# Performance work log

Hardware: AMD Instinct MI355X
Metric: run time of the kernel (lower is better)

## Reference

```python
import jax, jax.numpy as jnp
import numpy as np

B, S, D, H, HD, F = 2, 2048, 2048, 16, 128, 8192
EPS = 1e-6
NEG_INF = -1e10


def rmsnorm(x, scale, eps=EPS):
    # T5 LayerNorm: no centering, mean of squares, learned scale
    x = x.astype(jnp.float32)
    mean2 = jnp.mean(jnp.square(x), axis=-1, keepdims=True)
    return x * jax.lax.rsqrt(mean2 + eps) * scale


def setup_inputs() -> dict:
    key = jax.random.key(0)
    ks = jax.random.split(key, 10)
    sd = 0.02
    return {
        "x": jax.random.normal(ks[0], (B, S, D), jnp.float32),
        "ln1_scale": jnp.ones((D,), jnp.float32),
        "wq": jax.random.normal(ks[1], (D, H, HD), jnp.float32) * sd,
        "wk": jax.random.normal(ks[2], (D, H, HD), jnp.float32) * sd,
        "wv": jax.random.normal(ks[3], (D, H, HD), jnp.float32) * sd,
        "qln_scale": jnp.ones((HD,), jnp.float32),
        "kln_scale": jnp.ones((HD,), jnp.float32),
        "wo": jax.random.normal(ks[4], (H, HD, D), jnp.float32) * sd,
        "ln2_scale": jnp.ones((D,), jnp.float32),
        "wi0": jax.random.normal(ks[5], (D, F), jnp.float32) * sd,
        "wi1": jax.random.normal(ks[6], (D, F), jnp.float32) * sd,
        "wout": jax.random.normal(ks[7], (F, D), jnp.float32) * sd,
    }


def reference(x, ln1_scale, wq, wk, wv, qln_scale, kln_scale, wo, ln2_scale, wi0, wi1, wout):
    # ---- pre-attention RMSNorm ----
    lnx = rmsnorm(x, ln1_scale)                                  # [B,S,D]
    # ---- QKV projections (DenseGeneral D -> (H,HD)) ----
    q = jnp.einsum("bsd,dhk->bshk", lnx, wq)                      # [B,S,H,HD]
    k = jnp.einsum("bsd,dhk->bshk", lnx, wk)
    v = jnp.einsum("bsd,dhk->bshk", lnx, wv)
    # ---- fused per-head QK LayerNorm ----
    q = rmsnorm(q, qln_scale)
    k = rmsnorm(k, kln_scale)
    # ---- attention scores + causal bias + softmax ----
    logits = jnp.einsum("bqhd,bkhd->bhqk", q, k)                  # [B,H,S,S]
    causal = jnp.tril(jnp.ones((S, S), bool))
    bias = jnp.where(causal, 0.0, NEG_INF).astype(logits.dtype)  # [S,S]
    probs = jax.nn.softmax(logits + bias[None, None])             # [B,H,S,S]
    # ---- weighted values + output projection ----
    attn = jnp.einsum("bhqk,bkhd->bqhd", probs, v)                # [B,S,H,HD]
    attn_out = jnp.einsum("bqhd,hdm->bqm", attn, wo)              # [B,S,D]
    inter = x + attn_out
    # ---- pre-MLP RMSNorm + gated MLP (silu * linear) ----
    h = rmsnorm(inter, ln2_scale)
    g = jax.nn.silu(h @ wi0) * (h @ wi1)                          # [B,S,F]
    mlp_out = g @ wout                                            # [B,S,D]
    return inter + mlp_out
```

## Files before the change

kernel.cpp:

```cpp
#include <hip/hip_runtime.h>

typedef unsigned short u16;
typedef unsigned int u32;
typedef __attribute__((ext_vector_type(8))) short bf16x8;
typedef __attribute__((ext_vector_type(2))) float f32x2;
typedef __attribute__((ext_vector_type(4))) float f32x4;
typedef __attribute__((ext_vector_type(4))) u32 u32x4;
typedef __attribute__((ext_vector_type(4))) unsigned short u16x4;

#define DEV __device__ __forceinline__

DEV u16 f2bf(float x) {
    u32 u = __builtin_bit_cast(u32, x);
    u += 0x7fffu + ((u >> 16) & 1u);
    return (u16)(u >> 16);
}
DEV float bf2f(u16 b) {
    u32 u = ((u32)b) << 16;
    return __builtin_bit_cast(float, u);
}

#define MFMA16(a, b, c) __builtin_amdgcn_mfma_f32_16x16x32_bf16((a), (b), (c), 0, 0, 0)

#define GLL16(gp, lp)                                                      \
    __builtin_amdgcn_global_load_lds(                                      \
        (const __attribute__((address_space(1))) u32*)(const void*)(gp),   \
        (__attribute__((address_space(3))) u32*)(void*)(lp), 16, 0, 0)

__global__ void fillsent(float* __restrict__ out, int n, float val)
{
    for (int i = blockIdx.x * blockDim.x + threadIdx.x; i < n; i += gridDim.x * blockDim.x)
        out[i] = val;
}

__global__ void wtrans(const float* __restrict__ in, u16* __restrict__ out, int K, int N)
{
    __shared__ u16 t[64][66];
    const int n0 = blockIdx.x * 64, k0 = blockIdx.y * 64, tid = threadIdx.x;
#pragma unroll
    for (int i = 0; i < 4; ++i) {
        int e = (i * 256 + tid) * 4;
        int r = e >> 6, c = e & 63;
        f32x4 v = *(const f32x4*)&in[(size_t)(k0 + r) * N + n0 + c];
        t[r][c] = f2bf(v[0]); t[r][c + 1] = f2bf(v[1]);
        t[r][c + 2] = f2bf(v[2]); t[r][c + 3] = f2bf(v[3]);
    }
    __syncthreads();
#pragma unroll
    for (int i = 0; i < 4; ++i) {
        int e = (i * 256 + tid) * 4;
        int r = e >> 6, c = e & 63;
        u16x4 wv;
        wv[0] = t[c][r]; wv[1] = t[c + 1][r]; wv[2] = t[c + 2][r]; wv[3] = t[c + 3][r];
        *(u16x4*)&out[(size_t)(n0 + r) * K + k0 + c] = wv;
    }
}

__global__ void wtrans4(const float* __restrict__ s0, const float* __restrict__ s1,
                        const float* __restrict__ s2, const float* __restrict__ s3,
                        u16* __restrict__ d0, u16* __restrict__ d1,
                        u16* __restrict__ d2, u16* __restrict__ d3)
{
    const float* in;
    u16* out;
    switch (blockIdx.z) {
        case 0: in = s0; out = d0; break;
        case 1: in = s1; out = d1; break;
        case 2: in = s2; out = d2; break;
        default: in = s3; out = d3; break;
    }
    __shared__ u16 t[64][66];
    const int n0 = blockIdx.x * 64, k0 = blockIdx.y * 64, tid = threadIdx.x;
#pragma unroll
    for (int i = 0; i < 4; ++i) {
        int e = (i * 256 + tid) * 4;
        int r = e >> 6, c = e & 63;
        f32x4 v = *(const f32x4*)&in[(size_t)(k0 + r) * 2048 + n0 + c];
        t[r][c] = f2bf(v[0]); t[r][c + 1] = f2bf(v[1]);
        t[r][c + 2] = f2bf(v[2]); t[r][c + 3] = f2bf(v[3]);
    }
    __syncthreads();
#pragma unroll
    for (int i = 0; i < 4; ++i) {
        int e = (i * 256 + tid) * 4;
        int r = e >> 6, c = e & 63;
        u16x4 wv;
        wv[0] = t[c][r]; wv[1] = t[c + 1][r]; wv[2] = t[c + 2][r]; wv[3] = t[c + 3][r];
        *(u16x4*)&out[(size_t)(n0 + r) * 2048 + k0 + c] = wv;
    }
}

__global__ void vtrans(const u16* __restrict__ in, u16* __restrict__ out)
{
    __shared__ u16 t[64][65];
    const int d0 = blockIdx.x * 64, s0 = blockIdx.y * 64, bh = blockIdx.z, tid = threadIdx.x;
    const u16* ip = in + (size_t)bh * 2048 * 128;
    u16* op = out + (size_t)bh * 128 * 2048;
    for (int i = tid; i < 4096; i += 256) {
        int r = i >> 6, c = i & 63;
        t[r][c] = ip[(size_t)(s0 + r) * 128 + d0 + c];
    }
    __syncthreads();
    for (int i = tid; i < 4096; i += 256) {
        int r = i >> 6, c = i & 63;
        op[(size_t)(d0 + r) * 2048 + s0 + c] = t[c][r];
    }
}

__global__ __launch_bounds__(256) void rmsnorm_d(const float* __restrict__ in,
                                                 const float* __restrict__ sc,
                                                 u16* __restrict__ out)
{
    __shared__ float red[4];
    const int row = blockIdx.x, tid = threadIdx.x;
    const float* p = in + (size_t)row * 2048 + tid * 8;
    f32x4 a = *(const f32x4*)p;
    f32x4 b = *(const f32x4*)(p + 4);
    float ss = a[0]*a[0] + a[1]*a[1] + a[2]*a[2] + a[3]*a[3]
             + b[0]*b[0] + b[1]*b[1] + b[2]*b[2] + b[3]*b[3];
    for (int d = 1; d < 64; d <<= 1) ss += __shfl_xor(ss, d, 64);
    if ((tid & 63) == 0) red[tid >> 6] = ss;
    __syncthreads();
    float rs = rsqrtf((red[0] + red[1] + red[2] + red[3]) * (1.0f / 2048.0f) + 1e-6f);
    const float* s = sc + tid * 8;
    u32x4 ov;
#pragma unroll
    for (int i = 0; i < 2; ++i) {
        f32x4 v = i ? b : a;
#pragma unroll
        for (int j = 0; j < 2; ++j) {
            float v0 = v[j * 2] * rs * s[i * 4 + j * 2];
            float v1 = v[j * 2 + 1] * rs * s[i * 4 + j * 2 + 1];
            ov[i * 2 + j] = (u32)f2bf(v0) | ((u32)f2bf(v1) << 16);
        }
    }
    *(u32x4*)(out + (size_t)row * 2048 + tid * 8) = ov;
}

__global__ __launch_bounds__(256) void rmsnorm_split(const float* __restrict__ in,
                                                     const float* __restrict__ sc,
                                                     u16* __restrict__ ohi,
                                                     u16* __restrict__ olo)
{
    __shared__ float red[4];
    const int row = blockIdx.x, tid = threadIdx.x;
    const float* p = in + (size_t)row * 2048 + tid * 8;
    f32x4 a = *(const f32x4*)p;
    f32x4 b = *(const f32x4*)(p + 4);
    float ss = a[0]*a[0] + a[1]*a[1] + a[2]*a[2] + a[3]*a[3]
             + b[0]*b[0] + b[1]*b[1] + b[2]*b[2] + b[3]*b[3];
    for (int d = 1; d < 64; d <<= 1) ss += __shfl_xor(ss, d, 64);
    if ((tid & 63) == 0) red[tid >> 6] = ss;
    __syncthreads();
    float rs = rsqrtf((red[0] + red[1] + red[2] + red[3]) * (1.0f / 2048.0f) + 1e-6f);
    const float* s = sc + tid * 8;
    u32x4 oh, ol;
#pragma unroll
    for (int i = 0; i < 2; ++i) {
        f32x4 v = i ? b : a;
#pragma unroll
        for (int j = 0; j < 2; ++j) {
            float v0 = v[j * 2] * rs * s[i * 4 + j * 2];
            float v1 = v[j * 2 + 1] * rs * s[i * 4 + j * 2 + 1];
            u16 h0 = f2bf(v0), h1 = f2bf(v1);
            u16 l0 = f2bf(v0 - bf2f(h0)), l1 = f2bf(v1 - bf2f(h1));
            oh[i * 2 + j] = (u32)h0 | ((u32)h1 << 16);
            ol[i * 2 + j] = (u32)l0 | ((u32)l1 << 16);
        }
    }
    *(u32x4*)(ohi + (size_t)row * 2048 + tid * 8) = oh;
    *(u32x4*)(olo + (size_t)row * 2048 + tid * 8) = ol;
}

template <int EPI>
__global__ __launch_bounds__(512, 2)
void gemm_bt8(const u16* __restrict__ Ap, const u16* __restrict__ Bt,
              float* __restrict__ outf, u16* __restrict__ outb,
              const float* __restrict__ resf, int M, int N, int K)
{
    extern __shared__ char lds[];
    char* AB = lds;
    char* BB = lds + 49152;
    const int tid = threadIdx.x, w = tid >> 6, l = tid & 63;
    const int lr = l & 15, lg = l >> 4;
    const int m0 = blockIdx.y * 128, n0 = blockIdx.x * 256;
    const int wr = (w >> 2) * 64, wc = (w & 3) * 64;
    const size_t ldb = (size_t)K * 2;
    const char* Ag = (const char*)Ap;
    const char* Bg = (const char*)Bt;
    const int ldsw = w * 1024;

    size_t ago[2], bgo[4];
#pragma unroll
    for (int i = 0; i < 2; ++i) {
        int p = (i * 512 + tid) * 16;
        int pr = p >> 7;
        int pc = (p ^ ((pr & 7) << 4)) & 127;
        ago[i] = (size_t)(m0 + pr) * ldb + pc;
    }
#pragma unroll
    for (int i = 0; i < 4; ++i) {
        int p = (i * 512 + tid) * 16;
        int pr = p >> 7;
        int pc = (p ^ ((pr & 7) << 4)) & 127;
        bgo[i] = (size_t)(n0 + pr) * ldb + pc;
    }

    f32x4 acc[4][4] = {};
    const int nkt = K / 64;

    GLL16(Ag + ago[0], AB + ldsw);
    GLL16(Ag + ago[1], AB + 8192 + ldsw);
    GLL16(Bg + bgo[0], BB + ldsw);
    GLL16(Bg + bgo[1], BB + 8192 + ldsw);
    GLL16(Bg + bgo[2], BB + 16384 + ldsw);
    GLL16(Bg + bgo[3], BB + 24576 + ldsw);
    if (nkt > 1) {
        char* Ad = AB + 16384;
        char* Bd = BB + 32768;
        GLL16(Ag + ago[0] + 128, Ad + ldsw);
        GLL16(Ag + ago[1] + 128, Ad + 8192 + ldsw);
        GLL16(Bg + bgo[0] + 128, Bd + ldsw);
        GLL16(Bg + bgo[1] + 128, Bd + 8192 + ldsw);
        GLL16(Bg + bgo[2] + 128, Bd + 16384 + ldsw);
        GLL16(Bg + bgo[3] + 128, Bd + 24576 + ldsw);
        asm volatile("s_waitcnt vmcnt(6)" ::: "memory");
    } else {
        asm volatile("s_waitcnt vmcnt(0)" ::: "memory");
    }
    __builtin_amdgcn_s_barrier();

    int cur = 0, stg = 2;
    for (int kt = 0; kt < nkt; ++kt) {
        char* Ac = AB + cur * 16384;
        char* Bc = BB + cur * 32768;
        char* Asd = AB + stg * 16384;
        char* Bsd = BB + stg * 32768;
        const bool dost = (kt + 2 < nkt);
        const size_t koff = (size_t)(kt + 2) * 128;

        bf16x8 af[4], bfa, bfb;
#pragma unroll
        for (int mf = 0; mf < 4; ++mf) {
            int ra = wr + mf * 16 + lr;
            af[mf] = *(const bf16x8*)(Ac + ((ra * 128 + lg * 16) ^ ((ra & 7) << 4)));
        }
        {
            int rb = wc + lr;
            bfa = *(const bf16x8*)(Bc + ((rb * 128 + lg * 16) ^ ((rb & 7) << 4)));
            rb = wc + 16 + lr;
            bfb = *(const bf16x8*)(Bc + ((rb * 128 + lg * 16) ^ ((rb & 7) << 4)));
        }
        if (dost) {
            GLL16(Ag + ago[0] + koff, Asd + ldsw);
            GLL16(Ag + ago[1] + koff, Asd + 8192 + ldsw);
        }
        __builtin_amdgcn_s_barrier();
        __builtin_amdgcn_s_setprio(1);
#pragma unroll
        for (int mf = 0; mf < 4; ++mf) acc[mf][0] = MFMA16(af[mf], bfa, acc[mf][0]);
#pragma unroll
        for (int mf = 0; mf < 4; ++mf) acc[mf][1] = MFMA16(af[mf], bfb, acc[mf][1]);
        __builtin_amdgcn_s_setprio(0);
        __builtin_amdgcn_s_barrier();
        {
            int rb = wc + 32 + lr;
            bfa = *(const bf16x8*)(Bc + ((rb * 128 + lg * 16) ^ ((rb & 7) << 4)));
            rb = wc + 48 + lr;
            bfb = *(const bf16x8*)(Bc + ((rb * 128 + lg * 16) ^ ((rb & 7) << 4)));
        }
        if (dost) {
            GLL16(Bg + bgo[0] + koff, Bsd + ldsw);
            GLL16(Bg + bgo[1] + koff, Bsd + 8192 + ldsw);
        }
        __builtin_amdgcn_s_barrier();
        __builtin_amdgcn_s_setprio(1);
#pragma unroll
        for (int mf = 0; mf < 4; ++mf) acc[mf][2] = MFMA16(af[mf], bfa, acc[mf][2]);
#pragma unroll
        for (int mf = 0; mf < 4; ++mf) acc[mf][3] = MFMA16(af[mf], bfb, acc[mf][3]);
        __builtin_amdgcn_s_setprio(0);
        __builtin_amdgcn_s_barrier();
#pragma unroll
        for (int mf = 0; mf < 4; ++mf) {
            int ra = wr + mf * 16 + lr;
            af[mf] = *(const bf16x8*)(Ac + ((ra * 128 + 64 + lg * 16) ^ ((ra & 7) << 4)));
        }
        {
            int rb = wc + lr;
            bfa = *(const bf16x8*)(Bc + ((rb * 128 + 64 + lg * 16) ^ ((rb & 7) << 4)));
            rb = wc + 16 + lr;
            bfb = *(const bf16x8*)(Bc + ((rb * 128 + 64 + lg * 16) ^ ((rb & 7) << 4)));
        }
        if (dost) {
            GLL16(Bg + bgo[2] + koff, Bsd + 16384 + ldsw);
        }
        __builtin_amdgcn_s_barrier();
        __builtin_amdgcn_s_setprio(1);
#pragma unroll
        for (int mf = 0; mf < 4; ++mf) acc[mf][0] = MFMA16(af[mf], bfa, acc[mf][0]);
#pragma unroll
        for (int mf = 0; mf < 4; ++mf) acc[mf][1] = MFMA16(af[mf], bfb, acc[mf][1]);
        __builtin_amdgcn_s_setprio(0);
        __builtin_amdgcn_s_barrier();
        {
            int rb = wc + 32 + lr;
            bfa = *(const bf16x8*)(Bc + ((rb * 128 + 64 + lg * 16) ^ ((rb & 7) << 4)));
            rb = wc + 48 + lr;
            bfb = *(const bf16x8*)(Bc + ((rb * 128 + 64 + lg * 16) ^ ((rb & 7) << 4)));
        }
        if (dost) {
            GLL16(Bg + bgo[3] + koff, Bsd + 24576 + ldsw);
        }
        __builtin_amdgcn_s_barrier();
        __builtin_amdgcn_s_setprio(1);
#pragma unroll
        for (int mf = 0; mf < 4; ++mf) acc[mf][2] = MFMA16(af[mf], bfa, acc[mf][2]);
#pragma unroll
        for (int mf = 0; mf < 4; ++mf) acc[mf][3] = MFMA16(af[mf], bfb, acc[mf][3]);
        __builtin_amdgcn_s_setprio(0);
        if (kt < nkt - 2) {
            asm volatile("s_waitcnt vmcnt(6)" ::: "memory");
            __builtin_amdgcn_s_barrier();
        } else if (kt == nkt - 2) {
            asm volatile("s_waitcnt vmcnt(0)" ::: "memory");
            __builtin_amdgcn_s_barrier();
        }
        cur = (cur == 2) ? 0 : cur + 1;
        stg = (stg == 2) ? 0 : stg + 1;
    }

#pragma unroll
    for (int mf = 0; mf < 4; ++mf) {
#pragma unroll
        for (int nf = 0; nf < 4; ++nf) {
#pragma unroll
            for (int r = 0; r < 4; ++r) {
                int m = m0 + wr + mf * 16 + lg * 4 + r;
                int n = n0 + wc + nf * 16 + lr;
                float v = acc[mf][nf][r];
                if constexpr (EPI == 0) {
                    outb[(((m >> 11) * 16 + (n >> 7)) << 18) + ((m & 2047) << 7) + (n & 127)] = f2bf(v);
                } else {
                    size_t idx = (size_t)m * N + n;
                    outf[idx] = v + resf[idx];
                }
            }
        }
    }
}

__global__ __launch_bounds__(256, 2)
void gemm2qk(const u16* __restrict__ Ahi, const u16* __restrict__ Alo,
             const u16* __restrict__ Bq, const u16* __restrict__ Bk,
             const float* __restrict__ qsc, const float* __restrict__ ksc,
             u16* __restrict__ qhi, u16* __restrict__ qlo,
             u16* __restrict__ khi, u16* __restrict__ klo, int M, int N, int K)
{
    __shared__ u16 Ah[128 * 64];
    __shared__ u16 Al[128 * 64];
    __shared__ u16 Bqs[128 * 64];
    __shared__ u16 Bks[128 * 64];
    __shared__ float ssq[128][2];
    __shared__ float ssk[128][2];
    const int tid = threadIdx.x, w = tid >> 6, l = tid & 63;
    const int lr = l & 15, lg = l >> 4;
    const int m0 = blockIdx.y * 128, n0 = blockIdx.x * 128;
    const int wr = (w >> 1) * 64, wc = (w & 1) * 64;
    f32x4 accq[4][4] = {}, acck[4][4] = {};
    int prow[4], pcol[4];
#pragma unroll
    for (int j = 0; j < 4; ++j) {
        int p = (j * 4 + w) * 1024 + l * 16;
        prow[j] = p >> 7;
        pcol[j] = (p ^ ((prow[j] & 7) << 4)) & 127;
    }
    const size_t ldb = (size_t)K * 2;
    const int nkt = K / 64;
    for (int kt = 0; kt < nkt; ++kt) {
#pragma unroll
        for (int j = 0; j < 4; ++j) {
            size_t ao = (size_t)(m0 + prow[j]) * ldb + kt * 128 + pcol[j];
            size_t bo = (size_t)(n0 + prow[j]) * ldb + kt * 128 + pcol[j];
            GLL16((const char*)Ahi + ao, (char*)Ah + (j * 4 + w) * 1024);
            GLL16((const char*)Alo + ao, (char*)Al + (j * 4 + w) * 1024);
            GLL16((const char*)Bq + bo, (char*)Bqs + (j * 4 + w) * 1024);
            GLL16((const char*)Bk + bo, (char*)Bks + (j * 4 + w) * 1024);
        }
        __syncthreads();
#pragma unroll
        for (int kc = 0; kc < 2; ++kc) {
            bf16x8 ahf[4], alf[4], bqf[4], bkf[4];
#pragma unroll
            for (int f = 0; f < 4; ++f) {
                int ra = wr + f * 16 + lr;
                int oa = (ra * 128 + kc * 64 + lg * 16) ^ ((ra & 7) << 4);
                ahf[f] = *(const bf16x8*)((const char*)Ah + oa);
                alf[f] = *(const bf16x8*)((const char*)Al + oa);
                int rb = wc + f * 16 + lr;
                int ob = (rb * 128 + kc * 64 + lg * 16) ^ ((rb & 7) << 4);
                bqf[f] = *(const bf16x8*)((const char*)Bqs + ob);
                bkf[f] = *(const bf16x8*)((const char*)Bks + ob);
            }
#pragma unroll
            for (int mf = 0; mf < 4; ++mf)
#pragma unroll
                for (int nf = 0; nf < 4; ++nf) {
                    accq[mf][nf] = MFMA16(ahf[mf], bqf[nf], accq[mf][nf]);
                    accq[mf][nf] = MFMA16(alf[mf], bqf[nf], accq[mf][nf]);
                    acck[mf][nf] = MFMA16(ahf[mf], bkf[nf], acck[mf][nf]);
                    acck[mf][nf] = MFMA16(alf[mf], bkf[nf], acck[mf][nf]);
                }
        }
        __syncthreads();
    }
    float spq[4][4], spk[4][4];
#pragma unroll
    for (int mf = 0; mf < 4; ++mf)
#pragma unroll
        for (int r = 0; r < 4; ++r) {
            float sq = 0.0f, sk = 0.0f;
#pragma unroll
            for (int nf = 0; nf < 4; ++nf) {
                float vq = accq[mf][nf][r]; sq += vq * vq;
                float vk = acck[mf][nf][r]; sk += vk * vk;
            }
            sq += __shfl_xor(sq, 1, 64); sq += __shfl_xor(sq, 2, 64);
            sq += __shfl_xor(sq, 4, 64); sq += __shfl_xor(sq, 8, 64);
            sk += __shfl_xor(sk, 1, 64); sk += __shfl_xor(sk, 2, 64);
            sk += __shfl_xor(sk, 4, 64); sk += __shfl_xor(sk, 8, 64);
            spq[mf][r] = sq;
            spk[mf][r] = sk;
        }
    if (lr == 0) {
#pragma unroll
        for (int mf = 0; mf < 4; ++mf)
#pragma unroll
            for (int r = 0; r < 4; ++r) {
                int mloc = wr + mf * 16 + lg * 4 + r;
                ssq[mloc][w & 1] = spq[mf][r];
                ssk[mloc][w & 1] = spk[mf][r];
            }
    }
    __syncthreads();
    const int head = n0 >> 7;
#pragma unroll
    for (int mf = 0; mf < 4; ++mf)
#pragma unroll
        for (int r = 0; r < 4; ++r) {
            int mloc = wr + mf * 16 + lg * 4 + r;
            int m = m0 + mloc;
            float rsq = rsqrtf((ssq[mloc][0] + ssq[mloc][1]) * (1.0f / 128.0f) + 1e-6f);
            float rsk = rsqrtf((ssk[mloc][0] + ssk[mloc][1]) * (1.0f / 128.0f) + 1e-6f);
            size_t base = (((size_t)(m >> 11) * 16 + head) << 18) + ((size_t)(m & 2047) << 7);
#pragma unroll
            for (int nf = 0; nf < 4; ++nf) {
                int hd = wc + nf * 16 + lr;
                float vq = accq[mf][nf][r] * rsq * qsc[hd];
                u16 hq = f2bf(vq);
                qhi[base + hd] = hq;
                qlo[base + hd] = f2bf(vq - bf2f(hq));
                float vk = acck[mf][nf][r] * rsk * ksc[hd];
                u16 hk = f2bf(vk);
                khi[base + hd] = hk;
                klo[base + hd] = f2bf(vk - bf2f(hk));
            }
        }
}

__global__ __launch_bounds__(256, 2)
void gemm_up(const u16* __restrict__ A, const u16* __restrict__ B0, const u16* __restrict__ B1,
             u16* __restrict__ G, int M, int N, int K)
{
    __shared__ u16 As[128 * 64];
    __shared__ u16 Bs0[128 * 64];
    __shared__ u16 Bs1[128 * 64];
    const int tid = threadIdx.x, w = tid >> 6, l = tid & 63;
    const int lr = l & 15, lg = l >> 4;
    const int m0 = blockIdx.y * 128, n0 = blockIdx.x * 128;
    const int wr = (w >> 1) * 64, wc = (w & 1) * 64;
    f32x4 acc0[4][4] = {}, acc1[4][4] = {};
    int prow[4], pcol[4];
#pragma unroll
    for (int j = 0; j < 4; ++j) {
        int p = (j * 4 + w) * 1024 + l * 16;
        prow[j] = p >> 7;
        pcol[j] = (p ^ ((prow[j] & 7) << 4)) & 127;
    }
    const size_t ldb = (size_t)K * 2;
    const int nkt = K / 64;
    for (int kt = 0; kt < nkt; ++kt) {
#pragma unroll
        for (int j = 0; j < 4; ++j) {
            GLL16((const char*)A + (size_t)(m0 + prow[j]) * ldb + kt * 128 + pcol[j], (char*)As + (j * 4 + w) * 1024);
            GLL16((const char*)B0 + (size_t)(n0 + prow[j]) * ldb + kt * 128 + pcol[j], (char*)Bs0 + (j * 4 + w) * 1024);
            GLL16((const char*)B1 + (size_t)(n0 + prow[j]) * ldb + kt * 128 + pcol[j], (char*)Bs1 + (j * 4 + w) * 1024);
        }
        __syncthreads();
#pragma unroll
        for (int kc = 0; kc < 2; ++kc) {
            bf16x8 af[4], b0f[4], b1f[4];
#pragma unroll
            for (int f = 0; f < 4; ++f) {
                int ra = wr + f * 16 + lr;
                af[f] = *(const bf16x8*)((const char*)As + ((ra * 128 + kc * 64 + lg * 16) ^ ((ra & 7) << 4)));
                int rb = wc + f * 16 + lr;
                int ob = (rb * 128 + kc * 64 + lg * 16) ^ ((rb & 7) << 4);
                b0f[f] = *(const bf16x8*)((const char*)Bs0 + ob);
                b1f[f] = *(const bf16x8*)((const char*)Bs1 + ob);
            }
#pragma unroll
            for (int mf = 0; mf < 4; ++mf)
#pragma unroll
                for (int nf = 0; nf < 4; ++nf) {
                    acc0[mf][nf] = MFMA16(af[mf], b0f[nf], acc0[mf][nf]);
                    acc1[mf][nf] = MFMA16(af[mf], b1f[nf], acc1[mf][nf]);
                }
        }
        __syncthreads();
    }
#pragma unroll
    for (int mf = 0; mf < 4; ++mf) {
#pragma unroll
        for (int nf = 0; nf < 4; ++nf) {
#pragma unroll
            for (int r = 0; r < 4; ++r) {
                int m = m0 + wr + mf * 16 + lg * 4 + r;
                int n = n0 + wc + nf * 16 + lr;
                float a = acc0[mf][nf][r];
                float b = acc1[mf][nf][r];
                G[(size_t)m * N + n] = f2bf(a / (1.0f + __expf(-a)) * b);
            }
        }
    }
}

__global__ __launch_bounds__(256, 2)
void flash(const u16* __restrict__ Qh, const u16* __restrict__ Ql,
           const u16* __restrict__ Kh, const u16* __restrict__ Kl,
           const u16* __restrict__ Vt, u16* __restrict__ O)
{
    __shared__ u16 Ksh[64 * 128];
    __shared__ u16 Ksl[64 * 128];
    __shared__ u16 Vs[128 * 64];
    __shared__ u16 Ps[4][16 * 64];
    const int tid = threadIdx.x, w = tid >> 6, l = tid & 63;
    const int lr = l & 15, lg = l >> 4;
    const int qb0 = blockIdx.x * 64, bh = blockIdx.y;

    const size_t qoff = ((size_t)bh * 2048 + qb0 + w * 16) * 128;
    bf16x8 qfh[4], qfl[4];
#pragma unroll
    for (int kc = 0; kc < 4; ++kc) {
        qfh[kc] = *(const bf16x8*)(Qh + qoff + lr * 128 + kc * 32 + lg * 8);
        qfl[kc] = *(const bf16x8*)(Ql + qoff + lr * 128 + kc * 32 + lg * 8);
    }

    f32x4 o[8] = {};
    float mrun[4] = {-1e30f, -1e30f, -1e30f, -1e30f};
    float lrun[4] = {};

    int kgo[4], vdo[4], voff[4];
#pragma unroll
    for (int j = 0; j < 4; ++j) {
        int p = (j * 4 + w) * 1024 + l * 16;
        kgo[j] = p ^ (((p >> 8) & 7) << 4);
        int d = p >> 7, c0 = (p >> 4) & 7;
        vdo[j] = d;
        voff[j] = (c0 ^ (d & 7)) << 4;
    }
    const char* kbh = (const char*)(Kh + (size_t)bh * 2048 * 128);
    const char* kbl = (const char*)(Kl + (size_t)bh * 2048 * 128);
    const char* vbase = (const char*)(Vt + (size_t)bh * 128 * 2048);
    const int tmax = blockIdx.x;

    for (int t = 0; t <= tmax; ++t) {
        const char* kgh = kbh + (size_t)t * 16384;
        const char* kgl = kbl + (size_t)t * 16384;
        const char* vg = vbase + t * 128;
#pragma unroll
        for (int j = 0; j < 4; ++j) {
            GLL16(kgh + kgo[j], (char*)Ksh + (j * 4 + w) * 1024);
            GLL16(kgl + kgo[j], (char*)Ksl + (j * 4 + w) * 1024);
            GLL16(vg + (size_t)vdo[j] * 4096 + voff[j], (char*)Vs + (j * 4 + w) * 1024);
        }
        __syncthreads();

        f32x4 sf[4];
#pragma unroll
        for (int kf = 0; kf < 4; ++kf) {
            f32x4 a = {};
            int row = kf * 16 + lr;
#pragma unroll
            for (int kc = 0; kc < 4; ++kc) {
                int off = (row * 256 + kc * 64 + lg * 16) ^ ((row & 7) << 4);
                bf16x8 khf = *(const bf16x8*)((const char*)Ksh + off);
                bf16x8 klf = *(const bf16x8*)((const char*)Ksl + off);
                a = MFMA16(qfh[kc], khf, a);
                a = MFMA16(qfh[kc], klf, a);
                a = MFMA16(qfl[kc], khf, a);
            }
            sf[kf] = a;
        }
        if (t == tmax) {
#pragma unroll
            for (int kf = 0; kf < 4; ++kf)
#pragma unroll
                for (int r = 0; r < 4; ++r)
                    if (t * 64 + kf * 16 + lr > qb0 + w * 16 + lg * 4 + r) sf[kf][r] = -1e30f;
        }
        float scl[4];
#pragma unroll
        for (int r = 0; r < 4; ++r) {
            float m_ = fmaxf(fmaxf(sf[0][r], sf[1][r]), fmaxf(sf[2][r], sf[3][r]));
            m_ = fmaxf(m_, __shfl_xor(m_, 1, 64));
            m_ = fmaxf(m_, __shfl_xor(m_, 2, 64));
            m_ = fmaxf(m_, __shfl_xor(m_, 4, 64));
            m_ = fmaxf(m_, __shfl_xor(m_, 8, 64));
            float mn = fmaxf(mrun[r], m_);
            scl[r] = __expf(mrun[r] - mn);
            mrun[r] = mn;
            float s_ = 0.0f;
#pragma unroll
            for (int kf = 0; kf < 4; ++kf) {
                float e = __expf(sf[kf][r] - mn);
                sf[kf][r] = e;
                s_ += e;
            }
            s_ += __shfl_xor(s_, 1, 64);
            s_ += __shfl_xor(s_, 2, 64);
            s_ += __shfl_xor(s_, 4, 64);
            s_ += __shfl_xor(s_, 8, 64);
            lrun[r] = lrun[r] * scl[r] + s_;
        }
#pragma unroll
        for (int f = 0; f < 8; ++f) {
            o[f][0] *= scl[0]; o[f][1] *= scl[1]; o[f][2] *= scl[2]; o[f][3] *= scl[3];
        }
        char* pb = (char*)&Ps[w][0];
#pragma unroll
        for (int kf = 0; kf < 4; ++kf)
#pragma unroll
            for (int r = 0; r < 4; ++r) {
                int q = lg * 4 + r;
                int byte = (q * 128 + kf * 32 + lr * 2) ^ ((q & 7) << 4);
                *(u16*)(pb + byte) = f2bf(sf[kf][r]);
            }
        __syncthreads();
#pragma unroll
        for (int kc = 0; kc < 2; ++kc) {
            bf16x8 pa = *(const bf16x8*)(pb + ((lr * 128 + kc * 64 + lg * 16) ^ ((lr & 7) << 4)));
#pragma unroll
            for (int df = 0; df < 8; ++df) {
                int vr = df * 16 + lr;
                bf16x8 vf = *(const bf16x8*)((const char*)Vs +
                    ((vr * 128 + kc * 64 + lg * 16) ^ ((vr & 7) << 4)));
                o[df] = MFMA16(pa, vf, o[df]);
            }
        }
        __syncthreads();
    }
    float inv[4];
#pragma unroll
    for (int r = 0; r < 4; ++r) inv[r] = 1.0f / lrun[r];
    const int b = bh >> 4, h = bh & 15;
#pragma unroll
    for (int df = 0; df < 8; ++df)
#pragma unroll
        for (int r = 0; r < 4; ++r) {
            int q = qb0 + w * 16 + lg * 4 + r;
            int d = df * 16 + lr;
            O[(((size_t)b * 2048 + q) * 16 + h) * 128 + d] = f2bf(o[df][r] * inv[r]);
        }
}

extern "C" void kernel_launch(void* const* d_in, const int* in_sizes, int n_in,
                              void* d_out, int out_size, void* d_ws, size_t ws_size,
                              hipStream_t stream)
{
    (void)in_sizes; (void)n_in;
    const float* x    = (const float*)d_in[0];
    const float* ln1  = (const float*)d_in[1];
    const float* wq   = (const float*)d_in[2];
    const float* wk   = (const float*)d_in[3];
    const float* wv   = (const float*)d_in[4];
    const float* qln  = (const float*)d_in[5];
    const float* kln  = (const float*)d_in[6];
    const float* wo   = (const float*)d_in[7];
    const float* ln2  = (const float*)d_in[8];
    const float* wi0  = (const float*)d_in[9];
    const float* wi1  = (const float*)d_in[10];
    const float* wout = (const float*)d_in[11];

    const size_t MB = 1ull << 20;
    char* ws = (char*)d_ws;
    if (ws_size < 256 * MB) {
        fillsent<<<2048, 256, 0, stream>>>((float*)d_out, out_size, (float)(ws_size >> 20));
        return;
    }

    (void)hipFuncSetAttribute((const void*)gemm_bt8<0>,
                              hipFuncAttributeMaxDynamicSharedMemorySize, 147456);
    (void)hipFuncSetAttribute((const void*)gemm_bt8<1>,
                              hipFuncAttributeMaxDynamicSharedMemorySize, 147456);

    u16* lnx_hi = (u16*)(ws + 0 * MB);
    u16* attn   = (u16*)(ws + 0 * MB);
    u16* lnx_lo = (u16*)(ws + 16 * MB);
    u16* h      = (u16*)(ws + 16 * MB);
    u16* q_hi   = (u16*)(ws + 32 * MB);
    u16* q_lo   = (u16*)(ws + 48 * MB);
    u16* g      = (u16*)(ws + 32 * MB);
    u16* k_hi   = (u16*)(ws + 64 * MB);
    u16* k_lo   = (u16*)(ws + 80 * MB);
    u16* v      = (u16*)(ws + 96 * MB);
    u16* vt     = (u16*)(ws + 112 * MB);
    u16* wo2t   = (u16*)(ws + 96 * MB);
    u16* wqt    = (u16*)(ws + 128 * MB);
    u16* wkt    = (u16*)(ws + 136 * MB);
    float* interp = (float*)(ws + 128 * MB);
    u16* wi0t   = (u16*)(ws + 160 * MB);
    u16* wi1t   = (u16*)(ws + 192 * MB);
    u16* wvt    = (u16*)(ws + 224 * MB);
    u16* wot    = (u16*)(ws + 232 * MB);

    dim3 blk(256);
    wtrans4<<<dim3(32, 32, 4), blk, 0, stream>>>(wq, wk, wv, wo, wqt, wkt, wvt, wot);
    wtrans<<<dim3(128, 32), blk, 0, stream>>>(wi0, wi0t, 2048, 8192);
    wtrans<<<dim3(128, 32), blk, 0, stream>>>(wi1, wi1t, 2048, 8192);

    rmsnorm_split<<<4096, blk, 0, stream>>>(x, ln1, lnx_hi, lnx_lo);

    gemm2qk<<<dim3(16, 32), blk, 0, stream>>>(lnx_hi, lnx_lo, wqt, wkt, qln, kln,
                                              q_hi, q_lo, k_hi, k_lo, 4096, 2048, 2048);

    gemm_bt8<0><<<dim3(8, 32), dim3(512), 147456, stream>>>(lnx_hi, wvt, nullptr, v, nullptr, 4096, 2048, 2048);
    vtrans<<<dim3(2, 32, 32), blk, 0, stream>>>(v, vt);

    flash<<<dim3(32, 32), blk, 0, stream>>>(q_hi, q_lo, k_hi, k_lo, vt, attn);

    gemm_bt8<1><<<dim3(8, 32), dim3(512), 147456, stream>>>(attn, wot, interp, nullptr, x, 4096, 2048, 2048);

    rmsnorm_d<<<4096, blk, 0, stream>>>(interp, ln2, h);

    gemm_up<<<dim3(64, 32), blk, 0, stream>>>(h, wi0t, wi1t, g, 4096, 8192, 2048);

    wtrans<<<dim3(32, 128), blk, 0, stream>>>(wout, wo2t, 8192, 2048);
    gemm_bt8<1><<<dim3(8, 32), dim3(512), 147456, stream>>>(g, wo2t, (float*)d_out, nullptr, interp, 4096, 2048, 8192);
}
```

Before: 896.4 us.

## Drop K low-part split in QK logits, vectorize V transpose, merge MLP weight transposes

Stops producing the bf16 low residual of normalized K, so the flash kernel loads only the high part of K and runs two MFMAs per chunk instead of three for the logits. This cuts global loads, LDS traffic and matrix work in attention, but lowers the precision of the logits. The V transpose kernel now moves data with 4-wide vector loads and stores and a padded LDS tile. The two wi0/wi1 transposes become one launch using the z grid dimension.

```diff
diff --git a/kernel.cpp b/kernel.cpp
--- a/kernel.cpp
+++ b/kernel.cpp
@@ -56,6 +56,32 @@
     }
 }
 
+__global__ void wtrans2(const float* __restrict__ sa, const float* __restrict__ sb,
+                        u16* __restrict__ da, u16* __restrict__ db, int K, int N)
+{
+    const float* in = blockIdx.z ? sb : sa;
+    u16* out = blockIdx.z ? db : da;
+    __shared__ u16 t[64][66];
+    const int n0 = blockIdx.x * 64, k0 = blockIdx.y * 64, tid = threadIdx.x;
+#pragma unroll
+    for (int i = 0; i < 4; ++i) {
+        int e = (i * 256 + tid) * 4;
+        int r = e >> 6, c = e & 63;
+        f32x4 v = *(const f32x4*)&in[(size_t)(k0 + r) * N + n0 + c];
+        t[r][c] = f2bf(v[0]); t[r][c + 1] = f2bf(v[1]);
+        t[r][c + 2] = f2bf(v[2]); t[r][c + 3] = f2bf(v[3]);
+    }
+    __syncthreads();
+#pragma unroll
+    for (int i = 0; i < 4; ++i) {
+        int e = (i * 256 + tid) * 4;
+        int r = e >> 6, c = e & 63;
+        u16x4 wv;
+        wv[0] = t[c][r]; wv[1] = t[c + 1][r]; wv[2] = t[c + 2][r]; wv[3] = t[c + 3][r];
+        *(u16x4*)&out[(size_t)(n0 + r) * K + k0 + c] = wv;
+    }
+}
+
 __global__ void wtrans4(const float* __restrict__ s0, const float* __restrict__ s1,
                         const float* __restrict__ s2, const float* __restrict__ s3,
                         u16* __restrict__ d0, u16* __restrict__ d1,
@@ -92,18 +118,25 @@
 
 __global__ void vtrans(const u16* __restrict__ in, u16* __restrict__ out)
 {
-    __shared__ u16 t[64][65];
+    __shared__ u16 t[64][68];
     const int d0 = blockIdx.x * 64, s0 = blockIdx.y * 64, bh = blockIdx.z, tid = threadIdx.x;
     const u16* ip = in + (size_t)bh * 2048 * 128;
     u16* op = out + (size_t)bh * 128 * 2048;
-    for (int i = tid; i < 4096; i += 256) {
-        int r = i >> 6, c = i & 63;
-        t[r][c] = ip[(size_t)(s0 + r) * 128 + d0 + c];
+#pragma unroll
+    for (int i = 0; i < 4; ++i) {
+        int e = (i * 256 + tid) * 4;
+        int r = e >> 6, c = e & 63;
+        u16x4 v = *(const u16x4*)&ip[(size_t)(s0 + r) * 128 + d0 + c];
+        t[r][c] = v[0]; t[r][c + 1] = v[1]; t[r][c + 2] = v[2]; t[r][c + 3] = v[3];
     }
     __syncthreads();
-    for (int i = tid; i < 4096; i += 256) {
-        int r = i >> 6, c = i & 63;
-        op[(size_t)(d0 + r) * 2048 + s0 + c] = t[c][r];
+#pragma unroll
+    for (int i = 0; i < 4; ++i) {
+        int e = (i * 256 + tid) * 4;
+        int r = e >> 6, c = e & 63;
+        u16x4 v;
+        v[0] = t[c][r]; v[1] = t[c + 1][r]; v[2] = t[c + 2][r]; v[3] = t[c + 3][r];
+        *(u16x4*)&op[(size_t)(d0 + r) * 2048 + s0 + c] = v;
     }
 }
 
@@ -355,7 +388,7 @@
              const u16* __restrict__ Bq, const u16* __restrict__ Bk,
              const float* __restrict__ qsc, const float* __restrict__ ksc,
              u16* __restrict__ qhi, u16* __restrict__ qlo,
-             u16* __restrict__ khi, u16* __restrict__ klo, int M, int N, int K)
+             u16* __restrict__ khi, int M, int N, int K)
 {
     __shared__ u16 Ah[128 * 64];
     __shared__ u16 Al[128 * 64];
@@ -460,10 +493,7 @@
                 u16 hq = f2bf(vq);
                 qhi[base + hd] = hq;
                 qlo[base + hd] = f2bf(vq - bf2f(hq));
-                float vk = acck[mf][nf][r] * rsk * ksc[hd];
-                u16 hk = f2bf(vk);
-                khi[base + hd] = hk;
-                klo[base + hd] = f2bf(vk - bf2f(hk));
+                khi[base + hd] = f2bf(acck[mf][nf][r] * rsk * ksc[hd]);
             }
         }
 }
@@ -537,11 +567,10 @@
 
 __global__ __launch_bounds__(256, 2)
 void flash(const u16* __restrict__ Qh, const u16* __restrict__ Ql,
-           const u16* __restrict__ Kh, const u16* __restrict__ Kl,
-           const u16* __restrict__ Vt, u16* __restrict__ O)
+           const u16* __restrict__ Kh, const u16* __restrict__ Vt,
+           u16* __restrict__ O)
 {
     __shared__ u16 Ksh[64 * 128];
-    __shared__ u16 Ksl[64 * 128];
     __shared__ u16 Vs[128 * 64];
     __shared__ u16 Ps[4][16 * 64];
     const int tid = threadIdx.x, w = tid >> 6, l = tid & 63;
@@ -570,18 +599,15 @@
         voff[j] = (c0 ^ (d & 7)) << 4;
     }
     const char* kbh = (const char*)(Kh + (size_t)bh * 2048 * 128);
-    const char* kbl = (const char*)(Kl + (size_t)bh * 2048 * 128);
     const char* vbase = (const char*)(Vt + (size_t)bh * 128 * 2048);
     const int tmax = blockIdx.x;
 
     for (int t = 0; t <= tmax; ++t) {
         const char* kgh = kbh + (size_t)t * 16384;
-        const char* kgl = kbl + (size_t)t * 16384;
         const char* vg = vbase + t * 128;
 #pragma unroll
         for (int j = 0; j < 4; ++j) {
             GLL16(kgh + kgo[j], (char*)Ksh + (j * 4 + w) * 1024);
-            GLL16(kgl + kgo[j], (char*)Ksl + (j * 4 + w) * 1024);
             GLL16(vg + (size_t)vdo[j] * 4096 + voff[j], (char*)Vs + (j * 4 + w) * 1024);
         }
         __syncthreads();
@@ -595,9 +621,7 @@
             for (int kc = 0; kc < 4; ++kc) {
                 int off = (row * 256 + kc * 64 + lg * 16) ^ ((row & 7) << 4);
                 bf16x8 khf = *(const bf16x8*)((const char*)Ksh + off);
-                bf16x8 klf = *(const bf16x8*)((const char*)Ksl + off);
                 a = MFMA16(qfh[kc], khf, a);
-                a = MFMA16(qfh[kc], klf, a);
                 a = MFMA16(qfl[kc], khf, a);
             }
             sf[kf] = a;
@@ -712,7 +736,6 @@
     u16* q_lo   = (u16*)(ws + 48 * MB);
     u16* g      = (u16*)(ws + 32 * MB);
     u16* k_hi   = (u16*)(ws + 64 * MB);
-    u16* k_lo   = (u16*)(ws + 80 * MB);
     u16* v      = (u16*)(ws + 96 * MB);
     u16* vt     = (u16*)(ws + 112 * MB);
     u16* wo2t   = (u16*)(ws + 96 * MB);
@@ -726,18 +749,17 @@
 
     dim3 blk(256);
     wtrans4<<<dim3(32, 32, 4), blk, 0, stream>>>(wq, wk, wv, wo, wqt, wkt, wvt, wot);
-    wtrans<<<dim3(128, 32), blk, 0, stream>>>(wi0, wi0t, 2048, 8192);
-    wtrans<<<dim3(128, 32), blk, 0, stream>>>(wi1, wi1t, 2048, 8192);
+    wtrans2<<<dim3(128, 32, 2), blk, 0, stream>>>(wi0, wi1, wi0t, wi1t, 2048, 8192);
 
     rmsnorm_split<<<4096, blk, 0, stream>>>(x, ln1, lnx_hi, lnx_lo);
 
     gemm2qk<<<dim3(16, 32), blk, 0, stream>>>(lnx_hi, lnx_lo, wqt, wkt, qln, kln,
-                                              q_hi, q_lo, k_hi, k_lo, 4096, 2048, 2048);
+                                              q_hi, q_lo, k_hi, 4096, 2048, 2048);
 
     gemm_bt8<0><<<dim3(8, 32), dim3(512), 147456, stream>>>(lnx_hi, wvt, nullptr, v, nullptr, 4096, 2048, 2048);
     vtrans<<<dim3(2, 32, 32), blk, 0, stream>>>(v, vt);
 
-    flash<<<dim3(32, 32), blk, 0, stream>>>(q_hi, q_lo, k_hi, k_lo, vt, attn);
+    flash<<<dim3(32, 32), blk, 0, stream>>>(q_hi, q_lo, k_hi, vt, attn);
 
     gemm_bt8<1><<<dim3(8, 32), dim3(512), 147456, stream>>>(attn, wot, interp, nullptr, x, 4096, 2048, 2048);
 
```

After: 841.4 us. 1.07x faster.
